# Kernel tuning notes

Hardware: AMD Instinct MI355X
Metric: run time of the kernel (lower is better)

The kernel has to match this reference:

```python
import jax, jax.numpy as jnp
import numpy as np

K = 1024          # num_embeddings
D = 768           # embedding_dim
COMMIT = 0.25     # commitment_cost
PW = 0.1          # perplexity_weight


def setup_inputs() -> dict:
    key = jax.random.key(0)
    k1, k2 = jax.random.split(key)
    inputs = jax.random.normal(k1, (32, 2048, D), dtype=jnp.float32)
    weight = jax.random.normal(k2, (K, D), dtype=jnp.float32)  # codebook
    return {"inputs": inputs, "weight": weight}


def reference(inputs, weight):
    """Eval-mode forward of VectorQuantizerEMA (deterministic nearest-code lookup)."""
    in_shape = inputs.shape
    flat = inputs.reshape(-1, D)                       # [N, D]
    valid = jnp.linalg.norm(flat, axis=1) > 1e-6       # padding mask [N]
    maskf = valid.astype(flat.dtype)
    n_valid = maskf.sum()

    dist = (jnp.sum(flat * flat, axis=1, keepdims=True)
            + jnp.sum(weight * weight, axis=1)
            - 2.0 * flat @ weight.T)

    idx = jnp.argmin(dist, axis=1)                     # [N]
    min_d = jnp.min(dist, axis=1)                      # [N]
    idx = jnp.where(valid, idx, 0)
    min_d = jnp.where(valid, min_d, 0.0)

    q_flat = weight[idx] * maskf[:, None]              # zeros at padded rows
    quantized = q_flat.reshape(in_shape)
    quantized_st = inputs + jax.lax.stop_gradient(quantized - inputs)

    # commitment loss: MSE over valid rows only
    sq_err = jnp.sum((flat - jax.lax.stop_gradient(q_flat)) ** 2, axis=1)
    loss_commit = jnp.sum(maskf * sq_err) / (n_valid * D)

    # perplexity over valid assignments (one-hot mean == normalized counts)
    counts = jnp.zeros((K,), flat.dtype).at[idx].add(maskf)
    avg_probs = counts / n_valid
    perplexity = jnp.exp(-jnp.sum(avg_probs * jnp.log(avg_probs + 1e-10)))
    perplexity_loss = -jnp.log(perplexity + 1e-10)

    total_loss = COMMIT * loss_commit + PW * perplexity_loss

    indices = idx.reshape(in_shape[:-1])
    min_distances = min_d.reshape(in_shape[:-1])
    return quantized_st, total_loss, indices, min_distances, perplexity
```

## Files before the change

kernel.cpp:

```cpp
#include <hip/hip_runtime.h>
#include <hip/hip_bf16.h>
#include <math.h>

#define NROWS 65536
#define DDIM  768
#define KCODES 1024
#define NCB   8
#define BM    128
#define BK    128
#define KC    32
#define NCH   (DDIM / KC)
#define BK2   32
#define NCH2  (DDIM / BK2)
#define PANEL_USH (24 * 4096)
#define GAP_TAU  0.3f
#define FILT_TAU 0.6f
#define RGRID 2048
#define QGRID 2048

#define OUT_LOSS ((size_t)NROWS * DDIM)
#define OUT_IDX  (OUT_LOSS + 1)
#define OUT_MIND (OUT_IDX + NROWS)
#define OUT_PERP (OUT_MIND + NROWS)

#define WS_SUM    0
#define WS_NSUS   8
#define WS_NVAL   12
#define WS_COUNTS 256
#define WS_WSQ    (WS_COUNTS + 4*KCODES)
#define WS_XSQ    (WS_WSQ + 4*KCODES)
#define WS_ROWS   (WS_XSQ + 4*NROWS)
#define WS_ROWI   (WS_ROWS + 4*NROWS)
#define WS_SUSP   (WS_ROWI + 4*NROWS)
#define WS_PM1    (WS_SUSP + 4*NROWS)
#define WS_PM2    (WS_PM1 + (size_t)4*NROWS*NCB)
#define WS_PIDX   (WS_PM2 + (size_t)4*NROWS*NCB)
#define WS_END    (WS_PIDX + (size_t)4*NROWS*NCB)
#define WS_AF16   ((WS_END + 255) & ~(size_t)255)
#define WS_WF16   (WS_AF16 + (size_t)NROWS * DDIM * 2)
#define WS_END2   (WS_WF16 + (size_t)KCODES * DDIM * 2)

typedef __attribute__((ext_vector_type(8))) _Float16 half8;
typedef __attribute__((ext_vector_type(4))) float f32x4;

#define GLOAD16(gsrc, ldst) \
    __builtin_amdgcn_global_load_lds( \
        (const __attribute__((address_space(1))) unsigned int*)(gsrc), \
        (__attribute__((address_space(3))) unsigned int*)(ldst), 16, 0, 0)

template <typename T>
__device__ inline T waveRedAdd(T v) {
#pragma unroll
    for (int o = 32; o; o >>= 1) v += __shfl_xor(v, o);
    return v;
}

__device__ inline ushort f2h(float f) {
    union { _Float16 h; ushort u; } c;
    c.h = (_Float16)f;
    return c.u;
}

__global__ void k_init(float* counts, int* n_suspect, unsigned* n_valid, double* sum_sqerr) {
    const int t = threadIdx.x;
    if (t == 0) { *n_suspect = 0; *n_valid = 0u; *sum_sqerr = 0.0; }
    for (int k = t; k < KCODES; k += 256) counts[k] = 0.f;
}

__global__ __launch_bounds__(256) void k_wsq(const float* __restrict__ W, float* __restrict__ wsq) {
    const int k = blockIdx.x;
    const int t = threadIdx.x;
    const float* w = W + (size_t)k * DDIM;
    const float a = w[t], b = w[t + 256], c = w[t + 512];
    float s = a * a + b * b + c * c;
    s = waveRedAdd(s);
    __shared__ float p[4];
    if ((t & 63) == 0) p[t >> 6] = s;
    __syncthreads();
    if (t == 0) wsq[k] = (p[0] + p[1]) + (p[2] + p[3]);
}

__global__ __launch_bounds__(256) void k_xsq(const float* __restrict__ A, float* __restrict__ xsq) {
    const int wid = threadIdx.x >> 6, lane = threadIdx.x & 63;
    const int row = blockIdx.x * 4 + wid;
    const float* x = A + (size_t)row * DDIM;
    float s = 0.f;
#pragma unroll
    for (int j = 0; j < 3; ++j) {
        const float4 v = *(const float4*)(x + (lane + 64 * j) * 4);
        s += v.x * v.x + v.y * v.y + v.z * v.z + v.w * v.w;
    }
    s = waveRedAdd(s);
    if (lane == 0) xsq[row] = s;
}

#define ASLOTS (NROWS * (DDIM / 8))
#define TSLOTS ((NROWS + KCODES) * (DDIM / 8))
__global__ __launch_bounds__(192) void k_convert(
    const float* __restrict__ A, const float* __restrict__ W,
    ushort* __restrict__ Af16, ushort* __restrict__ Wf16,
    float* __restrict__ xsq)
{
    __shared__ float part[4];
    const int t = threadIdx.x;
    const int wv = t >> 6;

#pragma unroll 1
    for (size_t base = (size_t)blockIdx.x * 192; base < (size_t)TSLOTS; base += (size_t)gridDim.x * 192) {
        const size_t gidx = base + t;
        const bool isA = base < (size_t)ASLOTS;
        const float* src = isA ? A : W;
        ushort* dst = isA ? Af16 : Wf16;
        const int sid = (int)(gidx - (isA ? 0 : (size_t)ASLOTS));
        const int row = sid / 96;
        const int sl = sid - row * 96;
        const int ch = sl >> 2, s = sl & 3;
        const float* p = src + (size_t)row * DDIM + ch * 32 + s * 8;
        const float4 a = *(const float4*)p;
        const float4 b = *(const float4*)(p + 4);
        uint4 v;
        v.x = ((unsigned)f2h(a.y) << 16) | f2h(a.x);
        v.y = ((unsigned)f2h(a.w) << 16) | f2h(a.z);
        v.z = ((unsigned)f2h(b.y) << 16) | f2h(b.x);
        v.w = ((unsigned)f2h(b.w) << 16) | f2h(b.z);
        const size_t dsti = (size_t)(row >> 7) * PANEL_USH + ch * 4096
                          + (row & 127) * 32 + ((s ^ ((row >> 1) & 3)) << 3);
        *(uint4*)(dst + dsti) = v;

        if (isA) {
            float sq = a.x * a.x + a.y * a.y + a.z * a.z + a.w * a.w
                     + b.x * b.x + b.y * b.y + b.z * b.z + b.w * b.w;
            if (wv == 1) {
#pragma unroll
                for (int o = 16; o; o >>= 1) sq += __shfl_xor(sq, o);
            } else {
                sq = waveRedAdd(sq);
            }
            if (t == 0)   part[0] = sq;
            if (t == 64)  part[1] = sq;
            if (t == 96)  part[2] = sq;
            if (t == 128) part[3] = sq;
            __syncthreads();
            if (t == 0) {
                const int r0 = (int)(base / 96);
                xsq[r0]     = part[0] + part[1];
                xsq[r0 + 1] = part[2] + part[3];
            }
            __syncthreads();
        }
    }
}

__global__ __launch_bounds__(256, 4) void k_partials_g(
    const ushort* __restrict__ Af16, const ushort* __restrict__ Wf16,
    const float* __restrict__ wsq,
    float* __restrict__ pm1, float* __restrict__ pm2, int* __restrict__ pidx)
{
    __shared__ __align__(16) ushort lds[2 * 2 * BM * BK2];

    const int bid = blockIdx.x;
    const int rb = ((bid & 7) << 6) | (bid >> 6);
    const int cb = (bid >> 3) & 7;

    const int tid = threadIdx.x;
    const int wid = tid >> 6, lane = tid & 63;
    const int wr = wid >> 1, wc = wid & 1;
    const int l15 = lane & 15, g = lane >> 4;

    const ushort* Ap = Af16 + (size_t)rb * PANEL_USH;
    const ushort* Wp = Wf16 + (size_t)cb * PANEL_USH;

    int aoff[4], boff[4];
#pragma unroll
    for (int rt = 0; rt < 4; ++rt) {
        const int r = wr * 64 + rt * 16 + l15;
        aoff[rt] = r * 32 + ((g ^ ((r >> 1) & 3)) << 3);
        const int c = wc * 64 + rt * 16 + l15;
        boff[rt] = c * 32 + ((g ^ ((c >> 1) & 3)) << 3);
    }

    f32x4 acc[4][4];
#pragma unroll
    for (int rt = 0; rt < 4; ++rt)
#pragma unroll
        for (int ct = 0; ct < 4; ++ct) acc[rt][ct] = (f32x4)0.f;

    const int lseg = lane << 3;
    auto STAGE = [&](int ch, int b) {
        ushort* As = lds + b * 8192;
        ushort* Ws = As + 4096;
        const ushort* Asrc = Ap + ch * 4096;
        const ushort* Wsrc = Wp + ch * 4096;
        GLOAD16(Asrc + (wid << 9) + lseg,       (char*)As + (wid << 10));
        GLOAD16(Asrc + ((wid + 4) << 9) + lseg, (char*)As + ((wid + 4) << 10));
        GLOAD16(Wsrc + (wid << 9) + lseg,       (char*)Ws + (wid << 10));
        GLOAD16(Wsrc + ((wid + 4) << 9) + lseg, (char*)Ws + ((wid + 4) << 10));
    };

    STAGE(0, 0);
    STAGE(1, 1);
    asm volatile("s_waitcnt vmcnt(4)" ::: "memory");
    __builtin_amdgcn_s_barrier();

#pragma unroll 1
    for (int ch = 0; ch < NCH2; ++ch) {
        const int cur = ch & 1;
        const ushort* As = lds + cur * 8192;
        const ushort* Ws = As + 4096;
        half8 bf[4];
#pragma unroll
        for (int ct = 0; ct < 4; ++ct) bf[ct] = *(const half8*)(Ws + boff[ct]);
        __builtin_amdgcn_s_setprio(1);
#pragma unroll
        for (int rt = 0; rt < 4; ++rt) {
            const half8 af = *(const half8*)(As + aoff[rt]);
#pragma unroll
            for (int ct = 0; ct < 4; ++ct)
                acc[rt][ct] = __builtin_amdgcn_mfma_f32_16x16x32_f16(af, bf[ct], acc[rt][ct], 0, 0, 0);
        }
        __builtin_amdgcn_s_setprio(0);
        if (ch + 1 == NCH2) break;
        asm volatile("s_waitcnt lgkmcnt(0)" ::: "memory");
        __builtin_amdgcn_s_barrier();
        if (ch + 2 < NCH2) {
            STAGE(ch + 2, cur);
            asm volatile("s_waitcnt vmcnt(4)" ::: "memory");
        } else {
            asm volatile("s_waitcnt vmcnt(0)" ::: "memory");
        }
        __builtin_amdgcn_s_barrier();
    }
    __syncthreads();

    float wq[4];
#pragma unroll
    for (int ct = 0; ct < 4; ++ct) wq[ct] = wsq[cb * BK + wc * 64 + ct * 16 + l15];
    const int cbase = cb * BK + wc * 64 + l15;

    float* tm1 = (float*)lds;
    float* tm2 = tm1 + 256;
    int*   ti1 = (int*)(tm2 + 256);

#pragma unroll
    for (int rt = 0; rt < 4; ++rt) {
        float m1q[4], m2q[4]; int i1q[4];
#pragma unroll
        for (int q = 0; q < 4; ++q) { m1q[q] = INFINITY; m2q[q] = INFINITY; i1q[q] = 0x7fffffff; }
#pragma unroll
        for (int ct = 0; ct < 4; ++ct) {
            const int col = cbase + ct * 16;
#pragma unroll
            for (int q = 0; q < 4; ++q) {
                const float s = fmaf(-2.f, acc[rt][ct][q], wq[ct]);
                if (s < m1q[q]) { m2q[q] = m1q[q]; m1q[q] = s; i1q[q] = col; }
                else if (s < m2q[q]) m2q[q] = s;
            }
        }
#pragma unroll
        for (int msk = 1; msk <= 8; msk <<= 1) {
#pragma unroll
            for (int q = 0; q < 4; ++q) {
                const float om1 = __shfl_xor(m1q[q], msk);
                const float om2 = __shfl_xor(m2q[q], msk);
                const int   oi1 = __shfl_xor(i1q[q], msk);
                if (om1 < m1q[q] || (om1 == m1q[q] && oi1 < i1q[q])) {
                    m2q[q] = fminf(m1q[q], om2); m1q[q] = om1; i1q[q] = oi1;
                } else m2q[q] = fminf(m2q[q], om1);
            }
        }
        if (l15 == 0) {
#pragma unroll
            for (int q = 0; q < 4; ++q) {
                const int rl = wr * 64 + rt * 16 + g * 4 + q;
                tm1[rl * 2 + wc] = m1q[q];
                tm2[rl * 2 + wc] = m2q[q];
                ti1[rl * 2 + wc] = i1q[q];
            }
        }
    }
    __syncthreads();
    if (tid < BM) {
        float m1 = tm1[tid * 2], m2 = tm2[tid * 2]; int i1 = ti1[tid * 2];
        const float bm1 = tm1[tid * 2 + 1], bm2 = tm2[tid * 2 + 1]; const int bi = ti1[tid * 2 + 1];
        if (bm1 < m1 || (bm1 == m1 && bi < i1)) { m2 = fminf(m1, bm2); m1 = bm1; i1 = bi; }
        else m2 = fminf(m2, bm1);
        const size_t row = (size_t)rb * BM + tid;
        pm1[row * NCB + cb] = m1;
        pm2[row * NCB + cb] = m2;
        pidx[row * NCB + cb] = i1;
    }
}

__global__ __launch_bounds__(256, 2) void k_partials(
    const float* __restrict__ A, const float* __restrict__ W,
    const float* __restrict__ wsq,
    float* __restrict__ pm1, float* __restrict__ pm2, int* __restrict__ pidx)
{
    __shared__ __align__(16) ushort lds[2 * BM * KC];
    ushort* As = lds;
    ushort* Ws = lds + BM * KC;

    const int bid = blockIdx.x;
    const int rb = ((bid & 7) << 6) | (bid >> 6);
    const int cb = (bid >> 3) & 7;

    const int tid = threadIdx.x;
    const int wid = tid >> 6, lane = tid & 63;
    const int wr = wid >> 1, wc = wid & 1;
    const int l15 = lane & 15, g = lane >> 4;

    const float* Ab = A + (size_t)rb * BM * DDIM;
    const float* Wb = W + (size_t)cb * BK * DDIM;

    const int srow = tid >> 3;
    const int sk4  = (tid & 7) << 2;
    const int sg   = (tid & 7) >> 1;
    const int sh   = (tid & 1) << 2;

    int aOff[4], bOff[4];
#pragma unroll
    for (int rt = 0; rt < 4; ++rt) {
        const int r = wr * 64 + rt * 16 + l15;
        aOff[rt] = r * KC + ((g ^ ((r >> 1) & 3)) << 3);
        const int c = wc * 64 + rt * 16 + l15;
        bOff[rt] = c * KC + ((g ^ ((c >> 1) & 3)) << 3);
    }

    f32x4 acc[4][4];
#pragma unroll
    for (int rt = 0; rt < 4; ++rt)
#pragma unroll
        for (int ct = 0; ct < 4; ++ct) acc[rt][ct] = (f32x4)0.f;

    float4 av[4], wv[4];
#pragma unroll
    for (int i = 0; i < 4; ++i) {
        av[i] = *(const float4*)(Ab + (size_t)(srow + 32 * i) * DDIM + sk4);
        wv[i] = *(const float4*)(Wb + (size_t)(srow + 32 * i) * DDIM + sk4);
    }

#pragma unroll 1
    for (int ch = 0; ch < NCH; ++ch) {
        __syncthreads();
#pragma unroll
        for (int i = 0; i < 4; ++i) {
            const int r = srow + 32 * i;
            const int wsl = r * KC + ((sg ^ ((r >> 1) & 3)) << 3) + sh;
            ushort4 ua; ua.x = f2h(av[i].x); ua.y = f2h(av[i].y); ua.z = f2h(av[i].z); ua.w = f2h(av[i].w);
            *(ushort4*)(As + wsl) = ua;
            ushort4 uw; uw.x = f2h(wv[i].x); uw.y = f2h(wv[i].y); uw.z = f2h(wv[i].z); uw.w = f2h(wv[i].w);
            *(ushort4*)(Ws + wsl) = uw;
        }
        __syncthreads();
        if (ch + 1 < NCH) {
            const int d0 = (ch + 1) * KC + sk4;
#pragma unroll
            for (int i = 0; i < 4; ++i) {
                av[i] = *(const float4*)(Ab + (size_t)(srow + 32 * i) * DDIM + d0);
                wv[i] = *(const float4*)(Wb + (size_t)(srow + 32 * i) * DDIM + d0);
            }
        }
        half8 af[4], bf[4];
#pragma unroll
        for (int rt = 0; rt < 4; ++rt) af[rt] = *(const half8*)(As + aOff[rt]);
#pragma unroll
        for (int ct = 0; ct < 4; ++ct) bf[ct] = *(const half8*)(Ws + bOff[ct]);
#pragma unroll
        for (int rt = 0; rt < 4; ++rt)
#pragma unroll
            for (int ct = 0; ct < 4; ++ct)
                acc[rt][ct] = __builtin_amdgcn_mfma_f32_16x16x32_f16(af[rt], bf[ct], acc[rt][ct], 0, 0, 0);
    }

    float wq[4];
#pragma unroll
    for (int ct = 0; ct < 4; ++ct) wq[ct] = wsq[cb * BK + wc * 64 + ct * 16 + l15];
    const int cbase = cb * BK + wc * 64 + l15;

    __syncthreads();
    float* tm1 = (float*)lds;
    float* tm2 = tm1 + 256;
    int*   ti1 = (int*)(tm2 + 256);

#pragma unroll
    for (int rt = 0; rt < 4; ++rt) {
        float m1q[4], m2q[4]; int i1q[4];
#pragma unroll
        for (int q = 0; q < 4; ++q) { m1q[q] = INFINITY; m2q[q] = INFINITY; i1q[q] = 0x7fffffff; }
#pragma unroll
        for (int ct = 0; ct < 4; ++ct) {
            const int col = cbase + ct * 16;
#pragma unroll
            for (int q = 0; q < 4; ++q) {
                const float s = fmaf(-2.f, acc[rt][ct][q], wq[ct]);
                if (s < m1q[q]) { m2q[q] = m1q[q]; m1q[q] = s; i1q[q] = col; }
                else if (s < m2q[q]) m2q[q] = s;
            }
        }
#pragma unroll
        for (int msk = 1; msk <= 8; msk <<= 1) {
#pragma unroll
            for (int q = 0; q < 4; ++q) {
                const float om1 = __shfl_xor(m1q[q], msk);
                const float om2 = __shfl_xor(m2q[q], msk);
                const int   oi1 = __shfl_xor(i1q[q], msk);
                if (om1 < m1q[q] || (om1 == m1q[q] && oi1 < i1q[q])) {
                    m2q[q] = fminf(m1q[q], om2); m1q[q] = om1; i1q[q] = oi1;
                } else m2q[q] = fminf(m2q[q], om1);
            }
        }
        if (l15 == 0) {
#pragma unroll
            for (int q = 0; q < 4; ++q) {
                const int rl = wr * 64 + rt * 16 + g * 4 + q;
                tm1[rl * 2 + wc] = m1q[q];
                tm2[rl * 2 + wc] = m2q[q];
                ti1[rl * 2 + wc] = i1q[q];
            }
        }
    }
    __syncthreads();
    if (tid < BM) {
        float m1 = tm1[tid * 2], m2 = tm2[tid * 2]; int i1 = ti1[tid * 2];
        const float bm1 = tm1[tid * 2 + 1], bm2 = tm2[tid * 2 + 1]; const int bi = ti1[tid * 2 + 1];
        if (bm1 < m1 || (bm1 == m1 && bi < i1)) { m2 = fminf(m1, bm2); m1 = bm1; i1 = bi; }
        else m2 = fminf(m2, bm1);
        const size_t row = (size_t)rb * BM + tid;
        pm1[row * NCB + cb] = m1;
        pm2[row * NCB + cb] = m2;
        pidx[row * NCB + cb] = i1;
    }
}

__global__ __launch_bounds__(256) void k_merge(
    const float* __restrict__ pm1, const float* __restrict__ pm2, const int* __restrict__ pidx,
    float* __restrict__ row_s, int* __restrict__ row_idx,
    int* __restrict__ suspects, int* __restrict__ n_suspect)
{
    const int row = blockIdx.x * 256 + threadIdx.x;
    float m1 = INFINITY, m2 = INFINITY; int i1 = 0x7fffffff;
#pragma unroll
    for (int cb = 0; cb < NCB; ++cb) {
        const float bm1 = pm1[(size_t)row * NCB + cb];
        const float bm2 = pm2[(size_t)row * NCB + cb];
        const int   bi  = pidx[(size_t)row * NCB + cb];
        if (bm1 < m1 || (bm1 == m1 && bi < i1)) { m2 = fminf(m1, bm2); m1 = bm1; i1 = bi; }
        else m2 = fminf(m2, bm1);
    }
    row_s[row] = m1;
    row_idx[row] = i1;
    if (m2 - m1 < GAP_TAU) {
        const int p = atomicAdd(n_suspect, 1);
        suspects[p] = row;
    }
}

__global__ __launch_bounds__(256) void k_repair(
    const float* __restrict__ A, const float* __restrict__ W,
    const float* __restrict__ pm1,
    const int* __restrict__ suspects, const int* __restrict__ n_suspect,
    float* __restrict__ row_s, int* __restrict__ row_idx)
{
    __shared__ __align__(16) float xrow[DDIM];
    __shared__ double wbest[4]; __shared__ int wbi[4];
    __shared__ double xps[4];
    __shared__ int qcb[NCB];
    __shared__ int nq;
    const int ns = *n_suspect;
    const int tid = threadIdx.x;
    const int wid = tid >> 6, lane = tid & 63;
    const int sub = tid & 3;
    const int cq  = tid >> 2;

    for (int s = blockIdx.x; s < ns; s += gridDim.x) {
        const int row = suspects[s];
        __syncthreads();
        xrow[tid]       = A[(size_t)row * DDIM + tid];
        xrow[tid + 256] = A[(size_t)row * DDIM + tid + 256];
        xrow[tid + 512] = A[(size_t)row * DDIM + tid + 512];
        if (tid == 0) {
            float gmin = INFINITY;
#pragma unroll
            for (int cb = 0; cb < NCB; ++cb) gmin = fminf(gmin, pm1[(size_t)row * NCB + cb]);
            int n = 0;
#pragma unroll
            for (int cb = 0; cb < NCB; ++cb)
                if (pm1[(size_t)row * NCB + cb] <= gmin + FILT_TAU) qcb[n++] = cb;
            nq = n;
        }
        __syncthreads();

        double xp = 0.0;
        {
            double t;
            t = (double)xrow[tid];       xp = fma(t, t, xp);
            t = (double)xrow[tid + 256]; xp = fma(t, t, xp);
            t = (double)xrow[tid + 512]; xp = fma(t, t, xp);
        }
        xp = waveRedAdd(xp);
        if (lane == 0) xps[wid] = xp;

        double best = 1e300; int bi = 0x7fffffff;
        const int ncand = nq * BK;
        for (int base = 0; base < ncand; base += 64) {
            const int ci = base + cq;
            const bool act = ci < ncand;
            double d = 0.0; int k = 0x7fffffff;
            if (act) {
                k = qcb[ci >> 7] * BK + (ci & (BK - 1));
                const float* wr = W + (size_t)k * DDIM + (sub << 2);
                const float* xr = xrow + (sub << 2);
                double d0 = 0.0, d1 = 0.0;
                for (int i = 0; i < DDIM; i += 16) {
                    const float4 wv = *(const float4*)(wr + i);
                    const float4 xv = *(const float4*)(xr + i);
                    double t;
                    t = (double)xv.x - (double)wv.x; d0 = fma(t, t, d0);
                    t = (double)xv.y - (double)wv.y; d1 = fma(t, t, d1);
                    t = (double)xv.z - (double)wv.z; d0 = fma(t, t, d0);
                    t = (double)xv.w - (double)wv.w; d1 = fma(t, t, d1);
                }
                d = d0 + d1;
            }
            d += __shfl_xor(d, 1);
            d += __shfl_xor(d, 2);
            if (act && sub == 0) {
                if (d < best || (d == best && k < bi)) { best = d; bi = k; }
            }
        }
#pragma unroll
        for (int o = 32; o; o >>= 1) {
            const double ob = __shfl_xor(best, o);
            const int oi = __shfl_xor(bi, o);
            if (ob < best || (ob == best && oi < bi)) { best = ob; bi = oi; }
        }
        if (lane == 0) { wbest[wid] = best; wbi[wid] = bi; }
        __syncthreads();
        if (tid == 0) {
            double b = wbest[0]; int i1 = wbi[0];
#pragma unroll
            for (int w = 1; w < 4; ++w)
                if (wbest[w] < b || (wbest[w] == b && wbi[w] < i1)) { b = wbest[w]; i1 = wbi[w]; }
            row_idx[row] = i1;
            row_s[row] = (float)(b - (xps[0] + xps[1] + xps[2] + xps[3]));
        }
    }
}

__global__ __launch_bounds__(256) void k_quantize(
    const float* __restrict__ W,
    const float* __restrict__ xsq,
    const float* __restrict__ row_s, const int* __restrict__ row_idx,
    float* __restrict__ out, float* __restrict__ counts,
    unsigned int* __restrict__ n_valid, double* __restrict__ sum_sqerr)
{
    const int wid = threadIdx.x >> 6, lane = threadIdx.x & 63;
    __shared__ double s_sum[4];
    __shared__ unsigned s_val[4];
    double wsum = 0.0; unsigned wval = 0;

#pragma unroll 1
    for (int it = 0; it < NROWS / (QGRID * 4); ++it) {
        const int row = (it * QGRID + blockIdx.x) * 4 + wid;
        const float xs = xsq[row];
        const bool valid = xs > 1e-12f;
        const int idx = row_idx[row];
        const int idxm = valid ? idx : 0;
        const float* w = W + (size_t)idx * DDIM;
        float* oq = out + (size_t)row * DDIM;
#pragma unroll
        for (int j = 0; j < 3; ++j) {
            float4 wv = *(const float4*)(w + (lane + 64 * j) * 4);
            if (!valid) { wv.x = 0.f; wv.y = 0.f; wv.z = 0.f; wv.w = 0.f; }
            *(float4*)(oq + (lane + 64 * j) * 4) = wv;
        }
        if (lane == 0) {
            const float mind = xs + row_s[row];
            if (valid) {
                wsum += (double)mind;
                ++wval;
                atomicAdd(&counts[idxm], 1.0f);
            }
            out[OUT_IDX + row]  = (float)idxm;
            out[OUT_MIND + row] = valid ? mind : 0.f;
        }
    }

    if (lane == 0) { s_sum[wid] = wsum; s_val[wid] = wval; }
    __syncthreads();
    if (threadIdx.x == 0) {
        atomicAdd(sum_sqerr, s_sum[0] + s_sum[1] + s_sum[2] + s_sum[3]);
        atomicAdd(n_valid, s_val[0] + s_val[1] + s_val[2] + s_val[3]);
    }
}

__global__ __launch_bounds__(256) void k_final(
    const float* __restrict__ counts, const unsigned int* __restrict__ n_valid,
    const double* __restrict__ sum_sqerr, float* __restrict__ out)
{
    const int t = threadIdx.x;
    const float nv = (float)(*n_valid);
    double ent = 0.0;
    for (int k = t; k < KCODES; k += 256) {
        const float p = counts[k] / nv;
        ent += (double)(p * logf(p + 1e-10f));
    }
    ent = waveRedAdd(ent);
    __shared__ double ps[4];
    if ((t & 63) == 0) ps[t >> 6] = ent;
    __syncthreads();
    if (t == 0) {
        const double e = ps[0] + ps[1] + ps[2] + ps[3];
        const double perp = exp(-e);
        const double ploss = -log(perp + 1e-10);
        const double commit = *sum_sqerr / ((double)(*n_valid) * (double)DDIM);
        out[OUT_LOSS] = (float)(0.25 * commit + 0.1 * ploss);
        out[OUT_PERP] = (float)perp;
    }
}

extern "C" void kernel_launch(void* const* d_in, const int* in_sizes, int n_in,
                              void* d_out, int out_size, void* d_ws, size_t ws_size,
                              hipStream_t stream) {
    const float* A = (const float*)d_in[0];
    const float* W = (const float*)d_in[1];
    float* out = (float*)d_out;
    char* ws = (char*)d_ws;
    if (ws_size < (size_t)WS_END) return;

    double*   sum_sqerr = (double*)(ws + WS_SUM);
    int*      n_suspect = (int*)(ws + WS_NSUS);
    unsigned* n_valid   = (unsigned*)(ws + WS_NVAL);
    float*    counts    = (float*)(ws + WS_COUNTS);
    float*    wsq       = (float*)(ws + WS_WSQ);
    float*    xsq       = (float*)(ws + WS_XSQ);
    float*    row_s     = (float*)(ws + WS_ROWS);
    int*      row_idx   = (int*)(ws + WS_ROWI);
    int*      suspects  = (int*)(ws + WS_SUSP);
    float*    pm1       = (float*)(ws + WS_PM1);
    float*    pm2       = (float*)(ws + WS_PM2);
    int*      pidx      = (int*)(ws + WS_PIDX);
    ushort*   Af16      = (ushort*)(ws + WS_AF16);
    ushort*   Wf16      = (ushort*)(ws + WS_WF16);

    const bool big = ws_size >= (size_t)WS_END2;

    hipLaunchKernelGGL(k_init, dim3(1), dim3(256), 0, stream, counts, n_suspect, n_valid, sum_sqerr);
    hipLaunchKernelGGL(k_wsq, dim3(KCODES), dim3(256), 0, stream, W, wsq);
    if (big) {
        hipLaunchKernelGGL(k_convert, dim3(2048), dim3(192), 0, stream, A, W, Af16, Wf16, xsq);
        hipLaunchKernelGGL(k_partials_g, dim3((NROWS / BM) * NCB), dim3(256), 0, stream, Af16, Wf16, wsq, pm1, pm2, pidx);
    } else {
        hipLaunchKernelGGL(k_xsq, dim3(NROWS / 4), dim3(256), 0, stream, A, xsq);
        hipLaunchKernelGGL(k_partials, dim3((NROWS / BM) * NCB), dim3(256), 0, stream, A, W, wsq, pm1, pm2, pidx);
    }
    hipLaunchKernelGGL(k_merge, dim3(NROWS / 256), dim3(256), 0, stream, pm1, pm2, pidx, row_s, row_idx, suspects, n_suspect);
    hipLaunchKernelGGL(k_repair, dim3(RGRID), dim3(256), 0, stream, A, W, pm1, suspects, n_suspect, row_s, row_idx);
    hipLaunchKernelGGL(k_quantize, dim3(QGRID), dim3(256), 0, stream, W, xsq, row_s, row_idx, out, counts, n_valid, sum_sqerr);
    hipLaunchKernelGGL(k_final, dim3(1), dim3(256), 0, stream, counts, n_valid, sum_sqerr, out);
}
```

Baseline: 364.5 us.

## Fuse merge, repair and quantize into one per-block kernel; fold init into wsq

Merges the partial-min merge, suspect-row exact repair and quantize/output stages into a single kernel where each block owns 128 rows and keeps per-row min/index and its suspect list in shared memory. This drops the global row_s/row_idx/suspects arrays, the global suspect counter atomic, and three launches. The init kernel is folded into the codebook-norm kernel. In exchange, the repair work is no longer spread over a global grid, so blocks with many suspect rows serialize their repairs and load can become uneven across blocks.

```diff
diff --git a/kernel.cpp b/kernel.cpp
--- a/kernel.cpp
+++ b/kernel.cpp
@@ -15,8 +15,7 @@
 #define PANEL_USH (24 * 4096)
 #define GAP_TAU  0.3f
 #define FILT_TAU 0.6f
-#define RGRID 2048
-#define QGRID 2048
+#define MRQ_ROWS 128
 
 #define OUT_LOSS ((size_t)NROWS * DDIM)
 #define OUT_IDX  (OUT_LOSS + 1)
@@ -24,15 +23,11 @@
 #define OUT_PERP (OUT_MIND + NROWS)
 
 #define WS_SUM    0
-#define WS_NSUS   8
 #define WS_NVAL   12
 #define WS_COUNTS 256
 #define WS_WSQ    (WS_COUNTS + 4*KCODES)
 #define WS_XSQ    (WS_WSQ + 4*KCODES)
-#define WS_ROWS   (WS_XSQ + 4*NROWS)
-#define WS_ROWI   (WS_ROWS + 4*NROWS)
-#define WS_SUSP   (WS_ROWI + 4*NROWS)
-#define WS_PM1    (WS_SUSP + 4*NROWS)
+#define WS_PM1    (WS_XSQ + 4*NROWS)
 #define WS_PM2    (WS_PM1 + (size_t)4*NROWS*NCB)
 #define WS_PIDX   (WS_PM2 + (size_t)4*NROWS*NCB)
 #define WS_END    (WS_PIDX + (size_t)4*NROWS*NCB)
@@ -61,15 +56,15 @@
     return c.u;
 }
 
-__global__ void k_init(float* counts, int* n_suspect, unsigned* n_valid, double* sum_sqerr) {
-    const int t = threadIdx.x;
-    if (t == 0) { *n_suspect = 0; *n_valid = 0u; *sum_sqerr = 0.0; }
-    for (int k = t; k < KCODES; k += 256) counts[k] = 0.f;
-}
-
-__global__ __launch_bounds__(256) void k_wsq(const float* __restrict__ W, float* __restrict__ wsq) {
+__global__ __launch_bounds__(256) void k_wsq(const float* __restrict__ W, float* __restrict__ wsq,
+                                             float* __restrict__ counts,
+                                             unsigned* __restrict__ n_valid, double* __restrict__ sum_sqerr) {
     const int k = blockIdx.x;
     const int t = threadIdx.x;
+    if (t == 0) {
+        counts[k] = 0.f;
+        if (k == 0) { *n_valid = 0u; *sum_sqerr = 0.0; }
+    }
     const float* w = W + (size_t)k * DDIM;
     const float a = w[t], b = w[t + 256], c = w[t + 512];
     float s = a * a + b * b + c * c;
@@ -432,48 +427,58 @@
     }
 }
 
-__global__ __launch_bounds__(256) void k_merge(
+__global__ __launch_bounds__(256) void k_mrq(
+    const float* __restrict__ A, const float* __restrict__ W,
     const float* __restrict__ pm1, const float* __restrict__ pm2, const int* __restrict__ pidx,
-    float* __restrict__ row_s, int* __restrict__ row_idx,
-    int* __restrict__ suspects, int* __restrict__ n_suspect)
+    const float* __restrict__ xsq,
+    float* __restrict__ out, float* __restrict__ counts,
+    unsigned int* __restrict__ n_valid, double* __restrict__ sum_sqerr)
 {
-    const int row = blockIdx.x * 256 + threadIdx.x;
-    float m1 = INFINITY, m2 = INFINITY; int i1 = 0x7fffffff;
-#pragma unroll
-    for (int cb = 0; cb < NCB; ++cb) {
-        const float bm1 = pm1[(size_t)row * NCB + cb];
-        const float bm2 = pm2[(size_t)row * NCB + cb];
-        const int   bi  = pidx[(size_t)row * NCB + cb];
-        if (bm1 < m1 || (bm1 == m1 && bi < i1)) { m2 = fminf(m1, bm2); m1 = bm1; i1 = bi; }
-        else m2 = fminf(m2, bm1);
-    }
-    row_s[row] = m1;
-    row_idx[row] = i1;
-    if (m2 - m1 < GAP_TAU) {
-        const int p = atomicAdd(n_suspect, 1);
-        suspects[p] = row;
-    }
-}
-
-__global__ __launch_bounds__(256) void k_repair(
-    const float* __restrict__ A, const float* __restrict__ W,
-    const float* __restrict__ pm1,
-    const int* __restrict__ suspects, const int* __restrict__ n_suspect,
-    float* __restrict__ row_s, int* __restrict__ row_idx)
-{
+    __shared__ float l_rs[MRQ_ROWS];
+    __shared__ int   l_ri[MRQ_ROWS];
+    __shared__ int   l_susp[MRQ_ROWS];
+    __shared__ int   l_ns;
     __shared__ __align__(16) float xrow[DDIM];
     __shared__ double wbest[4]; __shared__ int wbi[4];
     __shared__ double xps[4];
     __shared__ int qcb[NCB];
     __shared__ int nq;
-    const int ns = *n_suspect;
+    __shared__ double s_sum[4];
+    __shared__ unsigned s_val[4];
+
     const int tid = threadIdx.x;
     const int wid = tid >> 6, lane = tid & 63;
+    const int row0 = blockIdx.x * MRQ_ROWS;
+
+    if (tid == 0) l_ns = 0;
+    __syncthreads();
+
+    if (tid < MRQ_ROWS) {
+        const size_t row = row0 + tid;
+        float m1 = INFINITY, m2 = INFINITY; int i1 = 0x7fffffff;
+#pragma unroll
+        for (int cb = 0; cb < NCB; ++cb) {
+            const float bm1 = pm1[row * NCB + cb];
+            const float bm2 = pm2[row * NCB + cb];
+            const int   bi  = pidx[row * NCB + cb];
+            if (bm1 < m1 || (bm1 == m1 && bi < i1)) { m2 = fminf(m1, bm2); m1 = bm1; i1 = bi; }
+            else m2 = fminf(m2, bm1);
+        }
+        l_rs[tid] = m1;
+        l_ri[tid] = i1;
+        if (m2 - m1 < GAP_TAU) {
+            const int p = atomicAdd(&l_ns, 1);
+            l_susp[p] = tid;
+        }
+    }
+    __syncthreads();
+
+    const int ns = l_ns;
     const int sub = tid & 3;
     const int cq  = tid >> 2;
-
-    for (int s = blockIdx.x; s < ns; s += gridDim.x) {
-        const int row = suspects[s];
+    for (int s = 0; s < ns; ++s) {
+        const int rl = l_susp[s];
+        const int row = row0 + rl;
         __syncthreads();
         xrow[tid]       = A[(size_t)row * DDIM + tid];
         xrow[tid + 256] = A[(size_t)row * DDIM + tid + 256];
@@ -541,30 +546,20 @@
 #pragma unroll
             for (int w = 1; w < 4; ++w)
                 if (wbest[w] < b || (wbest[w] == b && wbi[w] < i1)) { b = wbest[w]; i1 = wbi[w]; }
-            row_idx[row] = i1;
-            row_s[row] = (float)(b - (xps[0] + xps[1] + xps[2] + xps[3]));
-        }
-    }
-}
-
-__global__ __launch_bounds__(256) void k_quantize(
-    const float* __restrict__ W,
-    const float* __restrict__ xsq,
-    const float* __restrict__ row_s, const int* __restrict__ row_idx,
-    float* __restrict__ out, float* __restrict__ counts,
-    unsigned int* __restrict__ n_valid, double* __restrict__ sum_sqerr)
-{
-    const int wid = threadIdx.x >> 6, lane = threadIdx.x & 63;
-    __shared__ double s_sum[4];
-    __shared__ unsigned s_val[4];
+            l_ri[rl] = i1;
+            l_rs[rl] = (float)(b - (xps[0] + xps[1] + xps[2] + xps[3]));
+        }
+    }
+    __syncthreads();
+
     double wsum = 0.0; unsigned wval = 0;
-
 #pragma unroll 1
-    for (int it = 0; it < NROWS / (QGRID * 4); ++it) {
-        const int row = (it * QGRID + blockIdx.x) * 4 + wid;
+    for (int k = 0; k < MRQ_ROWS / 4; ++k) {
+        const int rl = wid * (MRQ_ROWS / 4) + k;
+        const int row = row0 + rl;
         const float xs = xsq[row];
         const bool valid = xs > 1e-12f;
-        const int idx = row_idx[row];
+        const int idx = l_ri[rl];
         const int idxm = valid ? idx : 0;
         const float* w = W + (size_t)idx * DDIM;
         float* oq = out + (size_t)row * DDIM;
@@ -575,7 +570,7 @@
             *(float4*)(oq + (lane + 64 * j) * 4) = wv;
         }
         if (lane == 0) {
-            const float mind = xs + row_s[row];
+            const float mind = xs + l_rs[rl];
             if (valid) {
                 wsum += (double)mind;
                 ++wval;
@@ -588,7 +583,7 @@
 
     if (lane == 0) { s_sum[wid] = wsum; s_val[wid] = wval; }
     __syncthreads();
-    if (threadIdx.x == 0) {
+    if (tid == 0) {
         atomicAdd(sum_sqerr, s_sum[0] + s_sum[1] + s_sum[2] + s_sum[3]);
         atomicAdd(n_valid, s_val[0] + s_val[1] + s_val[2] + s_val[3]);
     }
@@ -629,14 +624,10 @@
     if (ws_size < (size_t)WS_END) return;
 
     double*   sum_sqerr = (double*)(ws + WS_SUM);
-    int*      n_suspect = (int*)(ws + WS_NSUS);
     unsigned* n_valid   = (unsigned*)(ws + WS_NVAL);
     float*    counts    = (float*)(ws + WS_COUNTS);
     float*    wsq       = (float*)(ws + WS_WSQ);
     float*    xsq       = (float*)(ws + WS_XSQ);
-    float*    row_s     = (float*)(ws + WS_ROWS);
-    int*      row_idx   = (int*)(ws + WS_ROWI);
-    int*      suspects  = (int*)(ws + WS_SUSP);
     float*    pm1       = (float*)(ws + WS_PM1);
     float*    pm2       = (float*)(ws + WS_PM2);
     int*      pidx      = (int*)(ws + WS_PIDX);
@@ -645,8 +636,7 @@
 
     const bool big = ws_size >= (size_t)WS_END2;
 
-    hipLaunchKernelGGL(k_init, dim3(1), dim3(256), 0, stream, counts, n_suspect, n_valid, sum_sqerr);
-    hipLaunchKernelGGL(k_wsq, dim3(KCODES), dim3(256), 0, stream, W, wsq);
+    hipLaunchKernelGGL(k_wsq, dim3(KCODES), dim3(256), 0, stream, W, wsq, counts, n_valid, sum_sqerr);
     if (big) {
         hipLaunchKernelGGL(k_convert, dim3(2048), dim3(192), 0, stream, A, W, Af16, Wf16, xsq);
         hipLaunchKernelGGL(k_partials_g, dim3((NROWS / BM) * NCB), dim3(256), 0, stream, Af16, Wf16, wsq, pm1, pm2, pidx);
@@ -654,8 +644,6 @@
         hipLaunchKernelGGL(k_xsq, dim3(NROWS / 4), dim3(256), 0, stream, A, xsq);
         hipLaunchKernelGGL(k_partials, dim3((NROWS / BM) * NCB), dim3(256), 0, stream, A, W, wsq, pm1, pm2, pidx);
     }
-    hipLaunchKernelGGL(k_merge, dim3(NROWS / 256), dim3(256), 0, stream, pm1, pm2, pidx, row_s, row_idx, suspects, n_suspect);
-    hipLaunchKernelGGL(k_repair, dim3(RGRID), dim3(256), 0, stream, A, W, pm1, suspects, n_suspect, row_s, row_idx);
-    hipLaunchKernelGGL(k_quantize, dim3(QGRID), dim3(256), 0, stream, W, xsq, row_s, row_idx, out, counts, n_valid, sum_sqerr);
+    hipLaunchKernelGGL(k_mrq, dim3(NROWS / MRQ_ROWS), dim3(256), 0, stream, A, W, pm1, pm2, pidx, xsq, out, counts, n_valid, sum_sqerr);
     hipLaunchKernelGGL(k_final, dim3(1), dim3(256), 0, stream, counts, n_valid, sum_sqerr, out);
 }
```

Result: slower. 381.5 us (+4.7%).
